# Performance work log

Hardware: AMD Instinct MI355X
Metric: run time of the kernel (lower is better)

The kernel has to match this reference:

```python
import jax, jax.numpy as jnp
import numpy as np

U, D, B, E, H = 128, 256, 1024, 64, 8
EPS_LN = 1e-5
FS0 = 1.0 / 137.036


def _ln(h, g, b):
    m = h.mean(-1, keepdims=True)
    v = jnp.var(h, axis=-1, keepdims=True)
    return (h - m) * jax.lax.rsqrt(v + EPS_LN) * g + b


def setup_inputs() -> dict:
    key = jax.random.key(0)
    ks = iter(jax.random.split(key, 40))

    def n(shape, s=0.05):
        return jax.random.normal(next(ks), shape, jnp.float32) * s

    return dict(
        x=jax.random.normal(next(ks), (B, D), jnp.float32),
        fs=FS0 + n((U,), 0.001),                                   # fine_structure per universe
        dm=-0.1 * jnp.log(jax.random.uniform(next(ks), (U,), jnp.float32, 1e-6, 1.0)),  # Exp(0.1)
        W1=n((U, D, 256)), b1=n((U, 256)), g1=jnp.ones((U, 256), jnp.float32), be1=jnp.zeros((U, 256), jnp.float32),
        W2=n((U, 256, 128)), b2=n((U, 128)), g2=jnp.ones((U, 128), jnp.float32), be2=jnp.zeros((U, 128), jnp.float32),
        W3=n((U, 128, E)), b3=n((U, E)),
        Wr=n((U, E, E)), br=n((U, E)),
        Wa1=n((U, E, 32)), ba1=n((U, 32)),
        Wa2=n((U, 32, 16)), ba2=n((U, 16)),
        Wa3=n((U, 16, 1)), ba3=n((U, 1)),
        Wqkv=n((3 * E, E)), bqkv=n((3 * E,)), Wo=n((E, E)), bo=n((E,)),
        Wc1=n((U, U // 2)), bc1=n((U // 2,)),
        Wc2=n((U // 2, U // 4)), bc2=n((U // 4,)),
        Wc3=n((U // 4, 1)), bc3=n((1,)),
    )


def reference(x, fs, dm, W1, b1, g1, be1, W2, b2, g2, be2, W3, b3, Wr, br,
              Wa1, ba1, Wa2, ba2, Wa3, ba3, Wqkv, bqkv, Wo, bo,
              Wc1, bc1, Wc2, bc2, Wc3, bc3):
    # --- 128 universes batched as one axis (replaces Python loop over UniverseHypothesis) ---
    corr = fs / FS0  # fine-structure correction; x_scaled = x*corr folded into linear output
    h = jnp.einsum('bd,udh->buh', x, W1) * corr[None, :, None] + b1[None]
    h = jax.nn.relu(_ln(h, g1, be1))                     # Dropout(0.1) identity in eval
    h = jax.nn.relu(_ln(jnp.einsum('buh,uhk->buk', h, W2) + b2[None], g2, be2))
    enc = jnp.einsum('buh,uhk->buk', h, W3) + b3[None]   # [B,U,64]
    re = jnp.einsum('bue,uef->buf', enc, Wr) + br[None]
    dmi = jnp.tanh(dm[None, :, None] * jnp.sum(enc * enc, -1, keepdims=True))
    a = jax.nn.relu(jnp.einsum('bue,uef->buf', re + dmi * enc, Wa1) + ba1[None])
    a = jax.nn.relu(jnp.einsum('bue,uef->buf', a, Wa2) + ba2[None])
    scores = jax.nn.sigmoid(jnp.einsum('bue,uef->buf', a, Wa3) + ba3[None])[..., 0]  # [B,U]
    # --- dimensional coupling: MHA self-attention over universe axis (decoherence dropout = eval identity) ---
    b_, u_, e_ = enc.shape
    hd = e_ // H
    qkv = jnp.einsum('bue,fe->buf', enc, Wqkv) + bqkv
    q, k, v = jnp.split(qkv, 3, axis=-1)
    q = q.reshape(b_, u_, H, hd); k = k.reshape(b_, u_, H, hd); v = v.reshape(b_, u_, H, hd)
    attn = jax.nn.softmax(jnp.einsum('bqhd,bkhd->bhqk', q, k) / jnp.sqrt(jnp.float32(hd)), axis=-1)
    coupled = jnp.einsum('bhqk,bkhd->bqhd', attn, v).reshape(b_, u_, e_)
    coupled = jnp.einsum('bue,fe->buf', coupled, Wo) + bo   # computed as in torch, unused downstream
    attn_w = attn.mean(axis=1)                              # torch MHA averages heads -> [B,U,U]
    # --- consensus fusion ---
    cons = jax.nn.relu(scores @ Wc1 + bc1)
    cons = jax.nn.relu(cons @ Wc2 + bc2)
    cons = jax.nn.sigmoid(cons @ Wc3 + bc3)                 # [B,1]
    weighted = scores * attn_w.mean(axis=1)                 # mean over query dim
    mva = jnp.sum(weighted * cons, axis=-1, keepdims=True)  # [B,1]
    collapse = (cons > 0.95).astype(jnp.float32)
    std = jnp.std(scores, axis=-1, ddof=1, keepdims=True)   # torch.std is unbiased
    mean = jnp.mean(scores, axis=-1, keepdims=True)
    agree = 1.0 - std / (mean + 1e-8)
    n_active = jnp.sum(scores > 0.1, axis=-1).astype(jnp.float32)
    return (mva, collapse, agree, cons, attn_w.mean(), n_active)
```

## Files before the change

kernel.cpp:

```cpp
#include <hip/hip_runtime.h>
#include <math.h>


typedef float f32x4 __attribute__((ext_vector_type(4)));
typedef int   i32x4 __attribute__((ext_vector_type(4)));

__device__ __forceinline__ void mfma_bf16(f32x4& c, i32x4 a, i32x4 b) {
    asm("v_mfma_f32_16x16x32_bf16 %0, %1, %2, %0" : "+v"(c) : "v"(a), "v"(b));
}

__device__ __forceinline__ void gl_lds16(const void* g, void* l) {
    __builtin_amdgcn_global_load_lds(
        (const __attribute__((address_space(1))) unsigned int*)g,
        (__attribute__((address_space(3))) unsigned int*)l, 16, 0, 0);
}

__device__ __forceinline__ unsigned short f2bf(float v) {
    union { __bf16 b; unsigned short u; } cv;
    cv.b = (__bf16)v;
    return cv.u;
}

__global__ __launch_bounds__(256)
void prep_kernel(const float* __restrict__ W1, const float* __restrict__ W2,
                 const float* __restrict__ W3, const float* __restrict__ Wr,
                 const float* __restrict__ x, const float* __restrict__ Wqkv,
                 unsigned short* __restrict__ W1t, unsigned short* __restrict__ W2t,
                 unsigned short* __restrict__ W3t, unsigned short* __restrict__ Wrt,
                 unsigned short* __restrict__ xb, unsigned short* __restrict__ wqkvb)
{
    const int bid = blockIdx.x, t = threadIdx.x;
    if (bid >= 3456) {
        const float* src; unsigned short* dst; int base;
        if (bid >= 3584) { src = Wqkv; dst = wqkvb; base = (bid - 3584) * 2048 + t * 8; }
        else             { src = x;    dst = xb;    base = (bid - 3456) * 2048 + t * 8; }
        const float4 v0 = *(const float4*)(src + base);
        const float4 v1 = *(const float4*)(src + base + 4);
        __align__(16) unsigned short o[8];
        o[0]=f2bf(v0.x); o[1]=f2bf(v0.y); o[2]=f2bf(v0.z); o[3]=f2bf(v0.w);
        o[4]=f2bf(v1.x); o[5]=f2bf(v1.y); o[6]=f2bf(v1.z); o[7]=f2bf(v1.w);
        *(uint4*)(dst + base) = *(const uint4*)o;
        return;
    }
    const float* src; unsigned short* dst; int u, k0, n0, N, ktiles;
    if (bid < 2048)      { u = bid >> 4;        int tl = bid & 15;       k0 = (tl>>2)*64; n0 = (tl&3)*64; N=256; ktiles=8; src = W1 + (size_t)u*65536; dst = W1t + (size_t)u*65536; }
    else if (bid < 3072) { int b2 = bid - 2048; u = b2 >> 3; int tl = b2 & 7; k0 = (tl>>1)*64; n0 = (tl&1)*64; N=128; ktiles=8; src = W2 + (size_t)u*32768; dst = W2t + (size_t)u*32768; }
    else if (bid < 3328) { int b3 = bid - 3072; u = b3 >> 1; int tl = b3 & 1; k0 = tl*64;      n0 = 0;         N=64;  ktiles=4; src = W3 + (size_t)u*8192;  dst = W3t + (size_t)u*8192;  }
    else                 { u = bid - 3328;      k0 = 0; n0 = 0;                                 N=64;  ktiles=2; src = Wr + (size_t)u*4096;  dst = Wrt + (size_t)u*4096;  }

    __shared__ unsigned short tile[64 * 65];
    #pragma unroll
    for (int i = 0; i < 16; ++i) {
        const int e = i * 256 + t;
        const int kk = e >> 6, nn = e & 63;
        tile[kk * 65 + nn] = f2bf(src[(size_t)(k0 + kk) * N + n0 + nn]);
    }
    __syncthreads();
    #pragma unroll
    for (int i = 0; i < 16; ++i) {
        const int e = i * 256 + t;
        const int nn = e >> 6, kk = e & 63;
        const int n = n0 + nn, k = k0 + kk;
        dst[(size_t)(((n >> 4) * ktiles + (k >> 5)) * 512 + (n & 15) * 32 + (k & 31))] = tile[kk * 65 + nn];
    }
}

__global__ __launch_bounds__(256, 4)
void fused_mfma(const unsigned short* __restrict__ xb,
                const unsigned short* __restrict__ W1t, const unsigned short* __restrict__ W2t,
                const unsigned short* __restrict__ W3t, const unsigned short* __restrict__ Wrt,
                const float* __restrict__ fs, const float* __restrict__ dm,
                const float* __restrict__ b1, const float* __restrict__ g1, const float* __restrict__ be1,
                const float* __restrict__ b2, const float* __restrict__ g2, const float* __restrict__ be2,
                const float* __restrict__ b3, const float* __restrict__ br,
                const float* __restrict__ Wa1, const float* __restrict__ ba1,
                const float* __restrict__ Wa2, const float* __restrict__ ba2,
                const float* __restrict__ Wa3, const float* __restrict__ ba3,
                unsigned short* __restrict__ enc_bfg, float* __restrict__ scores_g)
{
    __shared__ __align__(128) char sm[39680];
    char* R0 = sm;
    float* pS = (float*)(sm + 36864);
    float* pQ = (float*)(sm + 37888);
    float2* rst = (float2*)(sm + 38912);
    float* dmis = (float*)(sm + 39424);

    const int t = threadIdx.x;
    const int wid = t >> 6, lane = t & 63, l15 = lane & 15, lk = lane >> 4;
    const int swz = (l15 & 7) << 4;
    const int lo64 = l15 * 64 + lk * 16;
    const int bx = blockIdx.x;
    const int xcd = bx & 7, idx = bx >> 3;
    const int u = ((idx >> 4) << 3) + xcd;
    const int b0 = (idx & 15) * 64;

    const float corru = fs[u] * 137.036f;
    const float dmu = dm[u];

    const char* xbase = (const char*)xb + (size_t)b0 * 512;
    const char* w1u = (const char*)W1t + (size_t)u * 131072;
    const char* w2u = (const char*)W2t + (size_t)u * 65536;
    const char* w3u = (const char*)W3t + (size_t)u * 16384;
    const char* wru = (const char*)Wrt + (size_t)u * 8192;

    #pragma unroll
    for (int it = 0; it < 8; ++it) {
        const int d = it * 4096 + t * 16;
        const int s = d ^ (((d >> 9) & 7) << 4);
        gl_lds16(xbase + s, R0 + it * 4096 + wid * 1024);
    }
    __syncthreads();

    const f32x4 z4 = {0.f, 0.f, 0.f, 0.f};
    f32x4 acc[4][4];
    #pragma unroll
    for (int mi = 0; mi < 4; ++mi)
        #pragma unroll
        for (int ni = 0; ni < 4; ++ni) acc[mi][ni] = z4;

    for (int p = 0; p < 4; ++p) {
        #pragma unroll
        for (int ks = 0; ks < 2; ++ks) {
            i32x4 af[4], bf[4];
            const int kt = p * 2 + ks;
            #pragma unroll
            for (int ni = 0; ni < 4; ++ni)
                bf[ni] = *(const i32x4*)(w1u + ((wid * 4 + ni) * 8 + kt) * 1024 + lo64);
            #pragma unroll
            for (int mi = 0; mi < 4; ++mi) {
                const int off = ((mi * 16 + l15) << 9) + p * 128 + ks * 64 + lk * 16;
                af[mi] = *(const i32x4*)(R0 + (off ^ swz));
            }
            #pragma unroll
            for (int mi = 0; mi < 4; ++mi)
                #pragma unroll
                for (int ni = 0; ni < 4; ++ni) mfma_bf16(acc[mi][ni], af[mi], bf[ni]);
        }
    }

    float bb[4], gg[4], ee[4];
    #pragma unroll
    for (int ni = 0; ni < 4; ++ni) {
        const int c = wid * 64 + ni * 16 + l15;
        bb[ni] = b1[u * 256 + c]; gg[ni] = g1[u * 256 + c]; ee[ni] = be1[u * 256 + c];
    }
    #pragma unroll
    for (int mi = 0; mi < 4; ++mi) {
        #pragma unroll
        for (int j = 0; j < 4; ++j) {
            float s = 0.f, q = 0.f;
            #pragma unroll
            for (int ni = 0; ni < 4; ++ni) {
                const float h = acc[mi][ni][j] * corru + bb[ni];
                acc[mi][ni][j] = h;
                s += h; q += h * h;
            }
            #pragma unroll
            for (int m = 1; m < 16; m <<= 1) { s += __shfl_xor(s, m); q += __shfl_xor(q, m); }
            if (l15 == 0) {
                const int r = mi * 16 + lk * 4 + j;
                pS[wid * 64 + r] = s; pQ[wid * 64 + r] = q;
            }
        }
    }
    __syncthreads();
    if (t < 64) {
        const float s = pS[t] + pS[64 + t] + pS[128 + t] + pS[192 + t];
        const float q = pQ[t] + pQ[64 + t] + pQ[128 + t] + pQ[192 + t];
        const float mean = s * (1.f / 256.f);
        const float var = fmaxf(q * (1.f / 256.f) - mean * mean, 0.f);
        rst[t] = make_float2(mean, rsqrtf(var + 1e-5f));
    }
    __syncthreads();
    #pragma unroll
    for (int mi = 0; mi < 4; ++mi) {
        #pragma unroll
        for (int j = 0; j < 4; ++j) {
            const int r = mi * 16 + lk * 4 + j;
            const float2 st = rst[r];
            #pragma unroll
            for (int ni = 0; ni < 4; ++ni) {
                const float h = fmaxf((acc[mi][ni][j] - st.x) * st.y * gg[ni] + ee[ni], 0.f);
                const int c = wid * 64 + ni * 16 + l15;
                const int off = (r << 9) + c * 2;
                *(__bf16*)(R0 + (off ^ ((r & 7) << 4))) = (__bf16)h;
            }
        }
    }
    __syncthreads();

    f32x4 acc2[4][2];
    #pragma unroll
    for (int mi = 0; mi < 4; ++mi) { acc2[mi][0] = z4; acc2[mi][1] = z4; }
    for (int p = 0; p < 4; ++p) {
        #pragma unroll
        for (int ks = 0; ks < 2; ++ks) {
            i32x4 af[4], bf2[2];
            const int kt = p * 2 + ks;
            #pragma unroll
            for (int ni = 0; ni < 2; ++ni)
                bf2[ni] = *(const i32x4*)(w2u + ((wid * 2 + ni) * 8 + kt) * 1024 + lo64);
            #pragma unroll
            for (int mi = 0; mi < 4; ++mi) {
                const int off = ((mi * 16 + l15) << 9) + p * 128 + ks * 64 + lk * 16;
                af[mi] = *(const i32x4*)(R0 + (off ^ swz));
            }
            #pragma unroll
            for (int mi = 0; mi < 4; ++mi)
                #pragma unroll
                for (int ni = 0; ni < 2; ++ni) mfma_bf16(acc2[mi][ni], af[mi], bf2[ni]);
        }
    }

    float bb2[2], gg2[2], ee2[2];
    #pragma unroll
    for (int ni = 0; ni < 2; ++ni) {
        const int c = wid * 32 + ni * 16 + l15;
        bb2[ni] = b2[u * 128 + c]; gg2[ni] = g2[u * 128 + c]; ee2[ni] = be2[u * 128 + c];
    }
    #pragma unroll
    for (int mi = 0; mi < 4; ++mi) {
        #pragma unroll
        for (int j = 0; j < 4; ++j) {
            float s = 0.f, q = 0.f;
            #pragma unroll
            for (int ni = 0; ni < 2; ++ni) {
                const float h = acc2[mi][ni][j] + bb2[ni];
                acc2[mi][ni][j] = h;
                s += h; q += h * h;
            }
            #pragma unroll
            for (int m = 1; m < 16; m <<= 1) { s += __shfl_xor(s, m); q += __shfl_xor(q, m); }
            if (l15 == 0) {
                const int r = mi * 16 + lk * 4 + j;
                pS[wid * 64 + r] = s; pQ[wid * 64 + r] = q;
            }
        }
    }
    __syncthreads();
    if (t < 64) {
        const float s = pS[t] + pS[64 + t] + pS[128 + t] + pS[192 + t];
        const float q = pQ[t] + pQ[64 + t] + pQ[128 + t] + pQ[192 + t];
        const float mean = s * (1.f / 128.f);
        const float var = fmaxf(q * (1.f / 128.f) - mean * mean, 0.f);
        rst[t] = make_float2(mean, rsqrtf(var + 1e-5f));
    }
    __syncthreads();
    #pragma unroll
    for (int mi = 0; mi < 4; ++mi) {
        #pragma unroll
        for (int j = 0; j < 4; ++j) {
            const int r = mi * 16 + lk * 4 + j;
            const float2 st = rst[r];
            #pragma unroll
            for (int ni = 0; ni < 2; ++ni) {
                const float h = fmaxf((acc2[mi][ni][j] - st.x) * st.y * gg2[ni] + ee2[ni], 0.f);
                const int c = wid * 32 + ni * 16 + l15;
                const int off = (r << 8) + c * 2;
                *(__bf16*)(R0 + (off ^ ((r & 7) << 4))) = (__bf16)h;
            }
        }
    }
    __syncthreads();

    f32x4 acc3[4];
    #pragma unroll
    for (int mi = 0; mi < 4; ++mi) acc3[mi] = z4;
    #pragma unroll
    for (int ks = 0; ks < 4; ++ks) {
        const i32x4 bfr = *(const i32x4*)(w3u + (wid * 4 + ks) * 1024 + lo64);
        #pragma unroll
        for (int mi = 0; mi < 4; ++mi) {
            const int off = ((mi * 16 + l15) << 8) + ks * 64 + lk * 16;
            const i32x4 afm = *(const i32x4*)(R0 + (off ^ swz));
            mfma_bf16(acc3[mi], afm, bfr);
        }
    }
    const int c16 = wid * 16 + l15;
    const float b3v = b3[u * 64 + c16];
    float encr[4][4];
    #pragma unroll
    for (int mi = 0; mi < 4; ++mi) {
        #pragma unroll
        for (int j = 0; j < 4; ++j) {
            const float e = acc3[mi][j] + b3v;
            encr[mi][j] = e;
            const int r = mi * 16 + lk * 4 + j;
            enc_bfg[((size_t)(b0 + r) * 128 + u) * 64 + c16] = f2bf(e);
            float q = e * e;
            #pragma unroll
            for (int m = 1; m < 16; m <<= 1) q += __shfl_xor(q, m);
            if (l15 == 0) pQ[wid * 64 + r] = q;
        }
    }
    __syncthreads();
    if (t < 64) {
        const float q = pQ[t] + pQ[64 + t] + pQ[128 + t] + pQ[192 + t];
        dmis[t] = tanhf(dmu * q);
    }
    #pragma unroll
    for (int mi = 0; mi < 4; ++mi) {
        #pragma unroll
        for (int j = 0; j < 4; ++j) {
            const int r = mi * 16 + lk * 4 + j;
            const int off = (r << 7) + c16 * 2;
            *(__bf16*)(R0 + (off ^ ((r & 7) << 4))) = (__bf16)encr[mi][j];
        }
    }
    __syncthreads();

    f32x4 accR[4];
    #pragma unroll
    for (int mi = 0; mi < 4; ++mi) accR[mi] = z4;
    #pragma unroll
    for (int ks = 0; ks < 2; ++ks) {
        const i32x4 bfr = *(const i32x4*)(wru + (wid * 2 + ks) * 1024 + lo64);
        #pragma unroll
        for (int mi = 0; mi < 4; ++mi) {
            const int off = ((mi * 16 + l15) << 7) + ks * 64 + lk * 16;
            const i32x4 afm = *(const i32x4*)(R0 + (off ^ swz));
            mfma_bf16(accR[mi], afm, bfr);
        }
    }
    const float brv = br[u * 64 + c16];
    #pragma unroll
    for (int mi = 0; mi < 4; ++mi) {
        #pragma unroll
        for (int j = 0; j < 4; ++j) {
            const int r = mi * 16 + lk * 4 + j;
            const float zv = accR[mi][j] + brv + dmis[r] * encr[mi][j];
            *(float*)(R0 + 8192 + r * 272 + c16 * 4) = zv;
        }
    }
    __syncthreads();

    #pragma unroll
    for (int it = 0; it < 2; ++it)
        gl_lds16((const char*)Wa1 + (size_t)u * 8192 + it * 4096 + t * 16,
                 R0 + it * 4096 + wid * 1024);
    if (t < 128)
        gl_lds16((const char*)Wa2 + (size_t)u * 2048 + t * 16, R0 + 25600 + wid * 1024);
    if (t < 16) ((float*)(R0 + 27648))[t] = Wa3[u * 16 + t];
    if (t == 16) ((float*)(R0 + 27648))[16] = ba3[u];
    __syncthreads();

    {
        const int row = t >> 2, g4 = t & 3;
        float accA[8] = {0.f,0.f,0.f,0.f,0.f,0.f,0.f,0.f};
        const float* zrow = (const float*)(R0 + 8192 + row * 272);
        const float* wa1s = (const float*)R0;
        for (int k = 0; k < 64; ++k) {
            const float zv = zrow[k];
            const float4 wA = *(const float4*)(wa1s + k * 32 + g4 * 8);
            const float4 wB = *(const float4*)(wa1s + k * 32 + g4 * 8 + 4);
            accA[0] += zv * wA.x; accA[1] += zv * wA.y; accA[2] += zv * wA.z; accA[3] += zv * wA.w;
            accA[4] += zv * wB.x; accA[5] += zv * wB.y; accA[6] += zv * wB.z; accA[7] += zv * wB.w;
        }
        const float4 bA = *(const float4*)(ba1 + u * 32 + g4 * 8);
        const float4 bB = *(const float4*)(ba1 + u * 32 + g4 * 8 + 4);
        float* a1s = (float*)(R0 + 28160);
        a1s[row * 34 + g4 * 8 + 0] = fmaxf(accA[0] + bA.x, 0.f);
        a1s[row * 34 + g4 * 8 + 1] = fmaxf(accA[1] + bA.y, 0.f);
        a1s[row * 34 + g4 * 8 + 2] = fmaxf(accA[2] + bA.z, 0.f);
        a1s[row * 34 + g4 * 8 + 3] = fmaxf(accA[3] + bA.w, 0.f);
        a1s[row * 34 + g4 * 8 + 4] = fmaxf(accA[4] + bB.x, 0.f);
        a1s[row * 34 + g4 * 8 + 5] = fmaxf(accA[5] + bB.y, 0.f);
        a1s[row * 34 + g4 * 8 + 6] = fmaxf(accA[6] + bB.z, 0.f);
        a1s[row * 34 + g4 * 8 + 7] = fmaxf(accA[7] + bB.w, 0.f);
    }
    __syncthreads();

    {
        const int row = t >> 2, g4 = t & 3;
        const float* a1s = (const float*)(R0 + 28160);
        const float* wa2s = (const float*)(R0 + 25600);
        float accB[4] = {0.f,0.f,0.f,0.f};
        for (int k = 0; k < 32; ++k) {
            const float av = a1s[row * 34 + k];
            const float4 w = *(const float4*)(wa2s + k * 16 + g4 * 4);
            accB[0] += av * w.x; accB[1] += av * w.y; accB[2] += av * w.z; accB[3] += av * w.w;
        }
        const float4 bB = *(const float4*)(ba2 + u * 16 + g4 * 4);
        float* a2s = (float*)R0;
        a2s[row * 18 + g4 * 4 + 0] = fmaxf(accB[0] + bB.x, 0.f);
        a2s[row * 18 + g4 * 4 + 1] = fmaxf(accB[1] + bB.y, 0.f);
        a2s[row * 18 + g4 * 4 + 2] = fmaxf(accB[2] + bB.z, 0.f);
        a2s[row * 18 + g4 * 4 + 3] = fmaxf(accB[3] + bB.w, 0.f);
    }
    __syncthreads();

    if (t < 64) {
        const float* a2s = (const float*)R0;
        const float* w3s = (const float*)(R0 + 27648);
        float a = w3s[16];
        #pragma unroll
        for (int k = 0; k < 16; ++k) a += a2s[t * 18 + k] * w3s[k];
        scores_g[(size_t)(b0 + t) * 128 + u] = 1.f / (1.f + __expf(-a));
    }
}

__global__ __launch_bounds__(256, 3)
void attn_kernel(const unsigned short* __restrict__ enc_bf,
                 const unsigned short* __restrict__ wqkv_bf,
                 const float* __restrict__ bqkv, float* __restrict__ smean,
                 float* __restrict__ bpart)
{
    __shared__ __align__(128) char sm[34944];
    char* Qp = sm;
    char* Ks = sm + 16384;
    float* colp = (float*)(sm + 32832);
    char* ENCs = sm;
    char* WQs  = sm + 16384;

    const int t = threadIdx.x;
    const int wid = t >> 6, lane = t & 63, l15 = lane & 15, lk = lane >> 4;
    const int swz = (l15 & 7) << 4;
    const int b = blockIdx.x;

    const char* eb = (const char*)(enc_bf + (size_t)b * 8192);
    #pragma unroll
    for (int it = 0; it < 4; ++it) {
        const int d = it * 4096 + t * 16;
        const int s = d ^ (((d >> 7) & 7) << 4);
        gl_lds16(eb + s, ENCs + it * 4096 + wid * 1024);
    }
    const char* wb = (const char*)wqkv_bf;
    #pragma unroll
    for (int it = 0; it < 4; ++it) {
        const int d = it * 4096 + t * 16;
        const int s = d ^ (((d >> 7) & 7) << 4);
        gl_lds16(wb + s, WQs + it * 4096 + wid * 1024);
    }
    __syncthreads();

    const f32x4 z4 = {0.f,0.f,0.f,0.f};
    f32x4 aq[2][4], ak[2][4];
    #pragma unroll
    for (int mi = 0; mi < 2; ++mi)
        #pragma unroll
        for (int ni = 0; ni < 4; ++ni) { aq[mi][ni] = z4; ak[mi][ni] = z4; }

    i32x4 af[2][2];
    #pragma unroll
    for (int mi = 0; mi < 2; ++mi)
        #pragma unroll
        for (int ks = 0; ks < 2; ++ks) {
            const int off = ((wid * 32 + mi * 16 + l15) << 7) + ks * 64 + lk * 16;
            af[mi][ks] = *(const i32x4*)(ENCs + (off ^ swz));
        }
    #pragma unroll
    for (int ni = 0; ni < 4; ++ni)
        #pragma unroll
        for (int ks = 0; ks < 2; ++ks) {
            const int offq = ((ni * 16 + l15) << 7) + ks * 64 + lk * 16;
            const i32x4 bq = *(const i32x4*)(WQs + (offq ^ swz));
            mfma_bf16(aq[0][ni], af[0][ks], bq);
            mfma_bf16(aq[1][ni], af[1][ks], bq);
            const i32x4 bk = *(const i32x4*)(WQs + ((offq + 8192) ^ swz));
            mfma_bf16(ak[0][ni], af[0][ks], bk);
            mfma_bf16(ak[1][ni], af[1][ks], bk);
        }

    float bqv[4], bkv[4];
    #pragma unroll
    for (int ni = 0; ni < 4; ++ni) {
        bqv[ni] = bqkv[ni * 16 + l15];
        bkv[ni] = bqkv[64 + ni * 16 + l15];
    }
    __syncthreads();

    {
        const int par = t >> 7, row = t & 127;
        char* base = Qp + par * 8192 + row * 64;
        *(f32x4*)(base + 16) = z4;
        *(f32x4*)(base + 32) = z4;
        *(f32x4*)(base + 48) = z4;
    }
    #pragma unroll
    for (int mi = 0; mi < 2; ++mi)
        #pragma unroll
        for (int ni = 0; ni < 4; ++ni)
            #pragma unroll
            for (int j = 0; j < 4; ++j) {
                const int row = wid * 32 + mi * 16 + lk * 4 + j;
                const int f = ni * 16 + l15;
                const int off = row * 128 + f * 2;
                *(__bf16*)(Ks + (off ^ ((row & 7) << 4))) = (__bf16)(ak[mi][ni][j] + bkv[ni]);
            }
    __syncthreads();

    const float qscale = 0.35355339059327373f;
    float cp[8] = {0.f,0.f,0.f,0.f,0.f,0.f,0.f,0.f};

    #pragma unroll
    for (int p = 0; p < 4; ++p) {
        #pragma unroll
        for (int mi = 0; mi < 2; ++mi)
            #pragma unroll
            for (int j = 0; j < 4; ++j) {
                const int row = wid * 32 + mi * 16 + lk * 4 + j;
                *(__bf16*)(Qp + (l15 >> 3) * 8192 + row * 64 + (l15 & 7) * 2) =
                    (__bf16)((aq[mi][p][j] + bqv[p]) * qscale);
            }
        __syncthreads();

        #pragma unroll 1
        for (int par = 0; par < 2; ++par) {
            const int h = p * 2 + par;
            const i32x4 aQ0 = *(const i32x4*)(Qp + par * 8192 + (wid * 32 + l15) * 64 + lk * 16);
            const i32x4 aQ1 = *(const i32x4*)(Qp + par * 8192 + (wid * 32 + 16 + l15) * 64 + lk * 16);
            f32x4 accS[2][8];
            #pragma unroll
            for (int ci = 0; ci < 8; ++ci) { accS[0][ci] = z4; accS[1][ci] = z4; }
            #pragma unroll
            for (int ci = 0; ci < 8; ++ci) {
                const int col = ci * 16 + l15;
                const i32x4 bK = *(const i32x4*)(Ks + ((col * 128 + ((h + lk) & 7) * 16) ^ ((col & 7) << 4)));
                mfma_bf16(accS[0][ci], aQ0, bK);
                mfma_bf16(accS[1][ci], aQ1, bK);
            }
            #pragma unroll
            for (int mi = 0; mi < 2; ++mi)
                #pragma unroll
                for (int j = 0; j < 4; ++j) {
                    float e[8];
                    float z = 0.f;
                    #pragma unroll
                    for (int ci = 0; ci < 8; ++ci) { e[ci] = __expf(accS[mi][ci][j]); z += e[ci]; }
                    z += __shfl_xor(z, 1); z += __shfl_xor(z, 2);
                    z += __shfl_xor(z, 4); z += __shfl_xor(z, 8);
                    const float zi = 1.f / z;
                    #pragma unroll
                    for (int ci = 0; ci < 8; ++ci) cp[ci] += e[ci] * zi;
                }
        }
        __syncthreads();
    }

    #pragma unroll
    for (int ci = 0; ci < 8; ++ci) {
        cp[ci] += __shfl_xor(cp[ci], 16);
        cp[ci] += __shfl_xor(cp[ci], 32);
    }
    if (lk == 0) {
        #pragma unroll
        for (int ci = 0; ci < 8; ++ci)
            colp[wid * 128 + ci * 16 + l15] = cp[ci];
    }
    __syncthreads();
    float v = 0.f;
    if (t < 128) {
        v = colp[t] + colp[128 + t] + colp[256 + t] + colp[384 + t];
        smean[(size_t)b * 128 + t] = v * (1.f / 1024.f);
    }
    #pragma unroll
    for (int m = 1; m < 64; m <<= 1) v += __shfl_xor(v, m);
    if (lane == 0) colp[512 + wid] = v;
    __syncthreads();
    if (t == 0)
        bpart[b] = (colp[512] + colp[513] + colp[514] + colp[515]) * (1.f / 1024.f);
}

__global__ __launch_bounds__(64)
void final_kernel(const float* __restrict__ scores_g, const float* __restrict__ smean,
                  const float* __restrict__ Wc1, const float* __restrict__ bc1,
                  const float* __restrict__ Wc2, const float* __restrict__ bc2,
                  const float* __restrict__ Wc3, const float* __restrict__ bc3,
                  float* __restrict__ out)
{
    __shared__ float sc[128];
    __shared__ float c1[64];
    __shared__ float c2[32];
    const int b = blockIdx.x, t = threadIdx.x;
    const float s0 = scores_g[(size_t)b * 128 + t];
    const float s1 = scores_g[(size_t)b * 128 + 64 + t];
    sc[t] = s0; sc[64 + t] = s1;
    const float v0 = smean[(size_t)b * 128 + t];
    const float v1 = smean[(size_t)b * 128 + 64 + t];
    __syncthreads();
    float a = bc1[t];
    #pragma unroll 8
    for (int i = 0; i < 128; ++i) a += sc[i] * Wc1[i * 64 + t];
    c1[t] = fmaxf(a, 0.f);
    __syncthreads();
    if (t < 32) {
        float a2 = bc2[t];
        #pragma unroll 8
        for (int i = 0; i < 64; ++i) a2 += c1[i] * Wc2[i * 32 + t];
        c2[t] = fmaxf(a2, 0.f);
    }
    __syncthreads();
    float p = (t < 32) ? c2[t] * Wc3[t] : 0.f;
    #pragma unroll
    for (int m = 1; m < 64; m <<= 1) p += __shfl_xor(p, m);
    const float cons = 1.f / (1.f + __expf(-(p + bc3[0])));

    float sum = s0 + s1;
    float sq  = s0 * s0 + s1 * s1;
    float wsm = s0 * v0 + s1 * v1;
    float na  = (s0 > 0.1f ? 1.f : 0.f) + (s1 > 0.1f ? 1.f : 0.f);
    #pragma unroll
    for (int m = 1; m < 64; m <<= 1) {
        sum += __shfl_xor(sum, m); sq += __shfl_xor(sq, m);
        wsm += __shfl_xor(wsm, m); na += __shfl_xor(na, m);
    }
    if (t == 0) {
        const float mean = sum * (1.f / 128.f);
        float var = (sq - 128.f * mean * mean) * (1.f / 127.f);
        var = fmaxf(var, 0.f);
        const float agree = 1.f - sqrtf(var) / (mean + 1e-8f);
        out[b]        = cons * wsm;
        out[1024 + b] = (cons > 0.95f) ? 1.f : 0.f;
        out[2048 + b] = agree;
        out[3072 + b] = cons;
        out[4097 + b] = na;
    }
}

__global__ __launch_bounds__(256)
void attnmean_kernel(const float* __restrict__ bpart, float* __restrict__ out)
{
    __shared__ float red[4];
    const int t = threadIdx.x;
    const int lane = t & 63, wid = t >> 6;
    float s = bpart[t] + bpart[256 + t] + bpart[512 + t] + bpart[768 + t];
    #pragma unroll
    for (int m = 1; m < 64; m <<= 1) s += __shfl_xor(s, m);
    if (lane == 0) red[wid] = s;
    __syncthreads();
    if (t == 0) out[4096] = (red[0] + red[1] + red[2] + red[3]) * (1.f / 131072.f);
}

extern "C" void kernel_launch(void* const* d_in, const int* in_sizes, int n_in,
                              void* d_out, int out_size, void* d_ws, size_t ws_size,
                              hipStream_t stream)
{
    const float* x    = (const float*)d_in[0];
    const float* fs   = (const float*)d_in[1];
    const float* dm   = (const float*)d_in[2];
    const float* W1   = (const float*)d_in[3];
    const float* b1   = (const float*)d_in[4];
    const float* g1   = (const float*)d_in[5];
    const float* be1  = (const float*)d_in[6];
    const float* W2   = (const float*)d_in[7];
    const float* b2   = (const float*)d_in[8];
    const float* g2   = (const float*)d_in[9];
    const float* be2  = (const float*)d_in[10];
    const float* W3   = (const float*)d_in[11];
    const float* b3   = (const float*)d_in[12];
    const float* Wr   = (const float*)d_in[13];
    const float* br   = (const float*)d_in[14];
    const float* Wa1  = (const float*)d_in[15];
    const float* ba1  = (const float*)d_in[16];
    const float* Wa2  = (const float*)d_in[17];
    const float* ba2  = (const float*)d_in[18];
    const float* Wa3  = (const float*)d_in[19];
    const float* ba3  = (const float*)d_in[20];
    const float* Wqkv = (const float*)d_in[21];
    const float* bqkv = (const float*)d_in[22];
    const float* Wc1  = (const float*)d_in[25];
    const float* bc1  = (const float*)d_in[26];
    const float* Wc2  = (const float*)d_in[27];
    const float* bc2  = (const float*)d_in[28];
    const float* Wc3  = (const float*)d_in[29];
    const float* bc3  = (const float*)d_in[30];

    float* out = (float*)d_out;
    char*  ws8 = (char*)d_ws;
    unsigned short* enc_bf = (unsigned short*)ws8;
    float* scores = (float*)(ws8 + 16777216);
    float* smean  = (float*)(ws8 + 17301504);
    float* bpart  = (float*)(ws8 + 17825792);
    unsigned short* xb    = (unsigned short*)(ws8 + 17829888);
    unsigned short* W1t   = (unsigned short*)(ws8 + 18354176);
    unsigned short* W2t   = (unsigned short*)(ws8 + 35131392);
    unsigned short* W3t   = (unsigned short*)(ws8 + 43520000);
    unsigned short* Wrt   = (unsigned short*)(ws8 + 45617152);
    unsigned short* wqkvb = (unsigned short*)(ws8 + 46665728);

    prep_kernel<<<3588, 256, 0, stream>>>(W1, W2, W3, Wr, x, Wqkv,
                                          W1t, W2t, W3t, Wrt, xb, wqkvb);
    fused_mfma<<<2048, 256, 0, stream>>>(xb, W1t, W2t, W3t, Wrt, fs, dm,
                                         b1, g1, be1, b2, g2, be2, b3, br,
                                         Wa1, ba1, Wa2, ba2, Wa3, ba3,
                                         enc_bf, scores);
    attn_kernel<<<1024, 256, 0, stream>>>(enc_bf, wqkvb, bqkv, smean, bpart);
    final_kernel<<<1024, 64, 0, stream>>>(scores, smean, Wc1, bc1, Wc2, bc2, Wc3, bc3, out);
    attnmean_kernel<<<1, 256, 0, stream>>>(bpart, out);
}
```

Before: 148.9 us.

## Double-buffer weight fragment loads and coalesce enc and score global stores

The first two MFMA GEMM loops now prefetch the next k-step's weight fragments into an alternating register buffer, so global load latency overlaps the current MFMAs. Encoder outputs are no longer written to global memory as scattered 2-byte stores. They are read back from the swizzled LDS tile and written as 16-byte vectors per row. Scores are stored universe-major so each block writes a contiguous run, and the final kernel reads them with a 1024 stride. The prefetch adds register pressure, and the final kernel's score reads become strided.

```diff
diff --git a/kernel.cpp b/kernel.cpp
--- a/kernel.cpp
+++ b/kernel.cpp
@@ -118,14 +118,21 @@
         #pragma unroll
         for (int ni = 0; ni < 4; ++ni) acc[mi][ni] = z4;
 
-    for (int p = 0; p < 4; ++p) {
-        #pragma unroll
-        for (int ks = 0; ks < 2; ++ks) {
-            i32x4 af[4], bf[4];
-            const int kt = p * 2 + ks;
-            #pragma unroll
-            for (int ni = 0; ni < 4; ++ni)
-                bf[ni] = *(const i32x4*)(w1u + ((wid * 4 + ni) * 8 + kt) * 1024 + lo64);
+    {
+        i32x4 bfP[4], bfQ[4];
+        #pragma unroll
+        for (int ni = 0; ni < 4; ++ni)
+            bfP[ni] = *(const i32x4*)(w1u + ((wid * 4 + ni) * 8 + 0) * 1024 + lo64);
+        #pragma unroll
+        for (int kt = 0; kt < 8; ++kt) {
+            if (kt < 7) {
+                #pragma unroll
+                for (int ni = 0; ni < 4; ++ni)
+                    ((kt & 1) ? bfP : bfQ)[ni] =
+                        *(const i32x4*)(w1u + ((wid * 4 + ni) * 8 + kt + 1) * 1024 + lo64);
+            }
+            i32x4 af[4];
+            const int p = kt >> 1, ks = kt & 1;
             #pragma unroll
             for (int mi = 0; mi < 4; ++mi) {
                 const int off = ((mi * 16 + l15) << 9) + p * 128 + ks * 64 + lk * 16;
@@ -134,7 +141,8 @@
             #pragma unroll
             for (int mi = 0; mi < 4; ++mi)
                 #pragma unroll
-                for (int ni = 0; ni < 4; ++ni) mfma_bf16(acc[mi][ni], af[mi], bf[ni]);
+                for (int ni = 0; ni < 4; ++ni)
+                    mfma_bf16(acc[mi][ni], af[mi], ((kt & 1) ? bfQ : bfP)[ni]);
         }
     }
 
@@ -192,14 +200,21 @@
     f32x4 acc2[4][2];
     #pragma unroll
     for (int mi = 0; mi < 4; ++mi) { acc2[mi][0] = z4; acc2[mi][1] = z4; }
-    for (int p = 0; p < 4; ++p) {
-        #pragma unroll
-        for (int ks = 0; ks < 2; ++ks) {
-            i32x4 af[4], bf2[2];
-            const int kt = p * 2 + ks;
-            #pragma unroll
-            for (int ni = 0; ni < 2; ++ni)
-                bf2[ni] = *(const i32x4*)(w2u + ((wid * 2 + ni) * 8 + kt) * 1024 + lo64);
+    {
+        i32x4 bfP[2], bfQ[2];
+        #pragma unroll
+        for (int ni = 0; ni < 2; ++ni)
+            bfP[ni] = *(const i32x4*)(w2u + ((wid * 2 + ni) * 8 + 0) * 1024 + lo64);
+        #pragma unroll
+        for (int kt = 0; kt < 8; ++kt) {
+            if (kt < 7) {
+                #pragma unroll
+                for (int ni = 0; ni < 2; ++ni)
+                    ((kt & 1) ? bfP : bfQ)[ni] =
+                        *(const i32x4*)(w2u + ((wid * 2 + ni) * 8 + kt + 1) * 1024 + lo64);
+            }
+            i32x4 af[4];
+            const int p = kt >> 1, ks = kt & 1;
             #pragma unroll
             for (int mi = 0; mi < 4; ++mi) {
                 const int off = ((mi * 16 + l15) << 9) + p * 128 + ks * 64 + lk * 16;
@@ -208,7 +223,8 @@
             #pragma unroll
             for (int mi = 0; mi < 4; ++mi)
                 #pragma unroll
-                for (int ni = 0; ni < 2; ++ni) mfma_bf16(acc2[mi][ni], af[mi], bf2[ni]);
+                for (int ni = 0; ni < 2; ++ni)
+                    mfma_bf16(acc2[mi][ni], af[mi], ((kt & 1) ? bfQ : bfP)[ni]);
         }
     }
 
@@ -285,12 +301,13 @@
         for (int j = 0; j < 4; ++j) {
             const float e = acc3[mi][j] + b3v;
             encr[mi][j] = e;
-            const int r = mi * 16 + lk * 4 + j;
-            enc_bfg[((size_t)(b0 + r) * 128 + u) * 64 + c16] = f2bf(e);
             float q = e * e;
             #pragma unroll
             for (int m = 1; m < 16; m <<= 1) q += __shfl_xor(q, m);
-            if (l15 == 0) pQ[wid * 64 + r] = q;
+            if (l15 == 0) {
+                const int r = mi * 16 + lk * 4 + j;
+                pQ[wid * 64 + r] = q;
+            }
         }
     }
     __syncthreads();
@@ -308,6 +325,17 @@
         }
     }
     __syncthreads();
+
+    {
+        const int c8 = t & 7;
+        #pragma unroll
+        for (int pass = 0; pass < 2; ++pass) {
+            const int row = pass * 32 + (t >> 3);
+            const int off = (row << 7) + c8 * 16;
+            const uint4 v = *(const uint4*)(R0 + (off ^ ((row & 7) << 4)));
+            *(uint4*)((char*)enc_bfg + (((size_t)(b0 + row) * 128 + u) << 7) + c8 * 16) = v;
+        }
+    }
 
     f32x4 accR[4];
     #pragma unroll
@@ -395,7 +423,7 @@
         float a = w3s[16];
         #pragma unroll
         for (int k = 0; k < 16; ++k) a += a2s[t * 18 + k] * w3s[k];
-        scores_g[(size_t)(b0 + t) * 128 + u] = 1.f / (1.f + __expf(-a));
+        scores_g[(size_t)u * 1024 + b0 + t] = 1.f / (1.f + __expf(-a));
     }
 }
 
@@ -572,8 +600,8 @@
     __shared__ float c1[64];
     __shared__ float c2[32];
     const int b = blockIdx.x, t = threadIdx.x;
-    const float s0 = scores_g[(size_t)b * 128 + t];
-    const float s1 = scores_g[(size_t)b * 128 + 64 + t];
+    const float s0 = scores_g[(size_t)t * 1024 + b];
+    const float s1 = scores_g[(size_t)(t + 64) * 1024 + b];
     sc[t] = s0; sc[64 + t] = s1;
     const float v0 = smean[(size_t)b * 128 + t];
     const float v1 = smean[(size_t)b * 128 + 64 + t];
```

After: 149.0 us. Within noise of the previous version (+0.1%).
